# Performance work log

Hardware: AMD Instinct MI355X
Metric: run time of the kernel (lower is better)

## Reference

```python
import jax, jax.numpy as jnp
import numpy as np

DIM = 1024
NUM_HEADS = 16
HEAD_DIM = DIM // NUM_HEADS
EPS = 1e-6


def rmsnorm(x, scale):
    # normalize over last dim (head_dim)
    ms = jnp.mean(x * x, axis=-1, keepdims=True)
    return scale * (x * jax.lax.rsqrt(ms + EPS))


def setup_inputs() -> dict:
    key = jax.random.key(0)
    ks = jax.random.split(key, 12)
    B, Nx, Nc = 2, 2048, 256
    std = 1.0 / np.sqrt(DIM)
    return {
        "x": jax.random.normal(ks[0], (B, Nx, DIM), jnp.float32),
        "c": jax.random.normal(ks[1], (B, Nc, DIM), jnp.float32),
        "w_qkv_x": jax.random.normal(ks[2], (DIM, 3 * DIM), jnp.float32) * std,
        "b_qkv_x": jnp.zeros((3 * DIM,), jnp.float32),
        "w_qkv_c": jax.random.normal(ks[3], (DIM, 3 * DIM), jnp.float32) * std,
        "b_qkv_c": jnp.zeros((3 * DIM,), jnp.float32),
        "s_q_x": jnp.ones((HEAD_DIM,), jnp.float32),
        "s_k_x": jnp.ones((HEAD_DIM,), jnp.float32),
        "s_q_c": jnp.ones((HEAD_DIM,), jnp.float32),
        "s_k_c": jnp.ones((HEAD_DIM,), jnp.float32),
        "w_proj_x": jax.random.normal(ks[4], (DIM, DIM), jnp.float32) * std,
        "b_proj_x": jnp.zeros((DIM,), jnp.float32),
        "w_proj_c": jax.random.normal(ks[5], (DIM, DIM), jnp.float32) * std,
        "b_proj_c": jnp.zeros((DIM,), jnp.float32),
    }


def reference(x, c, w_qkv_x, b_qkv_x, w_qkv_c, b_qkv_c,
              s_q_x, s_k_x, s_q_c, s_k_c,
              w_proj_x, b_proj_x, w_proj_c, b_proj_c):
    B, Nx, C = x.shape
    Nc = c.shape[1]
    H, D = NUM_HEADS, HEAD_DIM

    def split_qkv(t, w, b, n):
        qkv = (t @ w + b).reshape(B, n, 3, H, D)
        qkv = jnp.transpose(qkv, (2, 0, 3, 1, 4))  # [3, B, H, n, D]
        return qkv[0], qkv[1], qkv[2]

    q_x, k_x, v_x = split_qkv(x, w_qkv_x, b_qkv_x, Nx)
    q_c, k_c, v_c = split_qkv(c, w_qkv_c, b_qkv_c, Nc)

    q = jnp.concatenate([rmsnorm(q_x, s_q_x), rmsnorm(q_c, s_q_c)], axis=2)
    k = jnp.concatenate([rmsnorm(k_x, s_k_x), rmsnorm(k_c, s_k_c)], axis=2)
    v = jnp.concatenate([v_x, v_c], axis=2)

    scale = 1.0 / jnp.sqrt(jnp.asarray(D, q.dtype))
    scores = jnp.einsum("bhqd,bhkd->bhqk", q, k) * scale
    attn = jax.nn.softmax(scores, axis=-1)
    out = jnp.einsum("bhqk,bhkd->bhqd", attn, v)  # [B, H, Nx+Nc, D]
    out = jnp.transpose(out, (0, 2, 1, 3)).reshape(B, Nx + Nc, C)

    x_out = out[:, :Nx] @ w_proj_x + b_proj_x
    c_out = out[:, Nx:] @ w_proj_c + b_proj_c
    return x_out, c_out
```

## Files before the change

### kernel.cpp

```cpp
#include <hip/hip_runtime.h>
#include <stdint.h>

typedef __attribute__((ext_vector_type(4)))  float f32x4;
typedef __attribute__((ext_vector_type(2)))  float f32x2;
typedef __attribute__((ext_vector_type(16))) float f32x16;
typedef __attribute__((ext_vector_type(8)))  short s16x8;
typedef __attribute__((ext_vector_type(4)))  short s16x4;

constexpr int kDIM = 1024;
constexpr int kD   = 64;
constexpr int kNT  = 2304;

static __device__ __forceinline__ short f2bf(float f) {
  union { float f; uint32_t i; } x; x.f = f;
  uint32_t r = x.i + 0x7fffu + ((x.i >> 16) & 1u);
  return (short)(r >> 16);
}
static __device__ __forceinline__ uint32_t cvtpk(float lo, float hi) {
  uint32_t r;
  asm volatile("v_cvt_pk_bf16_f32 %0, %1, %2" : "=v"(r) : "v"(lo), "v"(hi));
  return r;
}
static __device__ __forceinline__ void gll16(const short* g, short* l) {
  __builtin_amdgcn_global_load_lds((const __attribute__((address_space(1))) void*)g,
                                   (__attribute__((address_space(3))) void*)l, 16, 0, 0);
}
#define FENCE() asm volatile("" ::: "memory")
#define WAITV8() asm volatile("s_waitcnt vmcnt(8)" ::: "memory")
#define WAITV4() asm volatile("s_waitcnt vmcnt(4)" ::: "memory")
#define WAITV0() asm volatile("s_waitcnt vmcnt(0)" ::: "memory")
#define WAITLGKM() do { asm volatile("s_waitcnt lgkmcnt(0)" ::: "memory"); \
                        __builtin_amdgcn_sched_barrier(0); } while (0)

__global__ __launch_bounds__(256) void k_cast2(const float* __restrict__ x,
                                               short* __restrict__ xb,
                                               const float* __restrict__ c,
                                               short* __restrict__ cb, int nxb) {
  int b = blockIdx.x;
  const float* in = x; short* out = xb;
  if (b >= nxb) { in = c; out = cb; b -= nxb; }
  int i = (b * 256 + threadIdx.x) * 4;
  f32x4 v = *(const f32x4*)(in + i);
  s16x4 o; o[0] = f2bf(v[0]); o[1] = f2bf(v[1]); o[2] = f2bf(v[2]); o[3] = f2bf(v[3]);
  *(s16x4*)(out + i) = o;
}

__global__ __launch_bounds__(256) void k_tcast2(const float* __restrict__ W0,
                                                short* __restrict__ Wt0,
                                                const float* __restrict__ W1,
                                                short* __restrict__ Wt1,
                                                int K, int N) {
  const float* W = blockIdx.z ? W1 : W0;
  short* Wt = blockIdx.z ? Wt1 : Wt0;
  __shared__ float tile[32][33];
  int n0 = blockIdx.x * 32, k0 = blockIdx.y * 32;
  int tx = threadIdx.x, ty = threadIdx.y;
#pragma unroll
  for (int i2 = 0; i2 < 4; ++i2) {
    int r = ty + 8 * i2;
    tile[r][tx] = W[(size_t)(k0 + r) * N + n0 + tx];
  }
  __syncthreads();
#pragma unroll
  for (int i2 = 0; i2 < 4; ++i2) {
    int r = ty + 8 * i2;
    Wt[(size_t)(n0 + r) * K + k0 + tx] = f2bf(tile[tx][r]);
  }
}

__global__ __launch_bounds__(256, 2) void k_gemm(
    const short* A0, const short* Wt0, const float* bias0,
    const float* sq0, const float* sk0,
    const short* A1, const short* Wt1, const float* bias1,
    const float* sq1, const float* sk1,
    short* outq, short* outk, short* outvt,
    float* outp0, float* outp1,
    int rpbs0, int arstride0, int aoff0, int posoff0,
    int rpbs1, int arstride1, int aoff1, int posoff1,
    int ybreak, int epi, int nx) {
  __shared__ __align__(16) short SH[32768];
  short* As0 = SH;          short* As1 = SH + 8192;
  short* Bs0 = SH + 16384;  short* Bs1 = SH + 24576;
  const int t = threadIdx.x;
  const int lane = t & 63, w = t >> 6;
  const int g = lane >> 4, r15 = lane & 15;
  const int wm = w >> 1, wn = w & 1;

  int lin = blockIdx.x;
  int xcd = lin & 7, kk = lin >> 3;
  int by = (xcd & 3) * 9 + kk % 9;
  int bx = (xcd >> 2) * (nx >> 1) + kk / 9;

  const short* A; const short* Wt; const float* bias;
  const float* sq; const float* sk; float* outp;
  int rpbs, arstride, aoff, posoff, my;
  if (by < ybreak) {
    A = A0; Wt = Wt0; bias = bias0; sq = sq0; sk = sk0; outp = outp0;
    rpbs = rpbs0; arstride = arstride0; aoff = aoff0; posoff = posoff0; my = by;
  } else {
    A = A1; Wt = Wt1; bias = bias1; sq = sq1; sk = sk1; outp = outp1;
    rpbs = rpbs1; arstride = arstride1; aoff = aoff1; posoff = posoff1; my = by - ybreak;
  }
  const int m0 = my * 128, n0 = bx * 128;

  const short* aptr[4]; const short* bptr[4];
  int wofs[4];
#pragma unroll
  for (int it = 0; it < 4; ++it) {
    int slot = t + 256 * it;
    int row = slot >> 3, gp = slot & 7;
    int gl = gp ^ (row & 7);
    int i = m0 + row;
    int arow = (i >> rpbs) * arstride + aoff + (i & ((1 << rpbs) - 1));
    aptr[it] = A + (size_t)arow * kDIM + 8 * gl;
    bptr[it] = Wt + (size_t)(n0 + row) * kDIM + 8 * gl;
    wofs[it] = (256 * it + 64 * w) * 8;
  }

  f32x4 acc[4][4] = {};

  auto STAGE = [&](short* Asd, short* Bsd) {
#pragma unroll
    for (int it = 0; it < 4; ++it) {
      gll16(aptr[it], Asd + wofs[it]);
      gll16(bptr[it], Bsd + wofs[it]);
      aptr[it] += 64; bptr[it] += 64;
    }
  };

  auto kstep = [&](const short* Ab, const short* Bb, short* Asd, short* Bsd,
                   bool last, bool pref) {
    if (last) WAITV0(); else WAITV8();
    __builtin_amdgcn_s_barrier();
    FENCE();
#pragma unroll
    for (int ks = 0; ks < 2; ++ks) {
      s16x8 af[4], bfr[4];
#pragma unroll
      for (int mf = 0; mf < 4; ++mf) {
        int row = wm * 64 + mf * 16 + r15;
        af[mf] = *(const s16x8*)(Ab + row * 64 + (((g + 4 * ks) ^ (row & 7)) * 8));
      }
#pragma unroll
      for (int nf = 0; nf < 4; ++nf) {
        int row = wn * 64 + nf * 16 + r15;
        bfr[nf] = *(const s16x8*)(Bb + row * 64 + (((g + 4 * ks) ^ (row & 7)) * 8));
      }
#pragma unroll
      for (int mf = 0; mf < 4; ++mf)
#pragma unroll
        for (int nf = 0; nf < 4; ++nf)
          acc[mf][nf] = __builtin_amdgcn_mfma_f32_16x16x32_bf16(af[mf], bfr[nf], acc[mf][nf], 0, 0, 0);
    }
    FENCE();
    __builtin_amdgcn_s_barrier();
    FENCE();
    if (pref) STAGE(Asd, Bsd);
  };

  STAGE(As0, Bs0);
  STAGE(As1, Bs1);
  for (int pp = 0; pp < 8; ++pp) {
    kstep(As0, Bs0, As0, Bs0, false,   pp < 7);
    kstep(As1, Bs1, As1, Bs1, pp == 7, pp < 7);
  }

  const int rpbm = (1 << rpbs) - 1;
  float* Ep = (float*)SH + w * 4096;

  if (epi == 1) {
#pragma unroll
    for (int mf = 0; mf < 4; ++mf)
#pragma unroll
      for (int nf = 0; nf < 4; ++nf) {
        f32x4 v = acc[mf][nf];
        float bj = bias[n0 + wn * 64 + nf * 16 + r15];
        int dl = nf * 16 + r15;
#pragma unroll
        for (int rg = 0; rg < 4; ++rg) {
          int r = mf * 16 + 4 * g + rg;
          Ep[r * 64 + (dl ^ ((r & 15) << 1))] = v[rg] + bj;
        }
      }
    WAITLGKM();
#pragma unroll
    for (int p2 = 0; p2 < 16; ++p2) {
      int r = 4 * p2 + (lane >> 4);
      int ch = lane & 15;
      int i = m0 + wm * 64 + r;
      f32x2 a = *(const f32x2*)&Ep[r * 64 + ((ch * 4) ^ ((r & 15) << 1))];
      f32x2 b2 = *(const f32x2*)&Ep[r * 64 + ((ch * 4 + 2) ^ ((r & 15) << 1))];
      f32x4 o; o[0] = a[0]; o[1] = a[1]; o[2] = b2[0]; o[3] = b2[1];
      *(f32x4*)(outp + (size_t)i * 1024 + n0 + wn * 64 + ch * 4) = o;
    }
    return;
  }

  const int eblk = (n0 + wn * 64) >> 10;
  const int hh = ((n0 + wn * 64) >> 6) & 15;
  if (eblk == 2) {
#pragma unroll
    for (int mf = 0; mf < 4; ++mf)
#pragma unroll
      for (int nf = 0; nf < 4; ++nf) {
        f32x4 v = acc[mf][nf];
        float bj = bias[n0 + wn * 64 + nf * 16 + r15];
        int dl = nf * 16 + r15;
#pragma unroll
        for (int rg = 0; rg < 4; ++rg) {
          int pin = mf * 16 + 4 * g + rg;
          int pp2 = (pin & 51) | ((pin & 4) << 1) | ((pin & 8) >> 1);
          Ep[dl * 64 + (pp2 ^ ((dl & 15) << 1))] = v[rg] + bj;
        }
      }
    WAITLGKM();
    int i0 = m0 + wm * 64;
    int b = i0 >> rpbs;
    int posb = (i0 & rpbm) + posoff;
#pragma unroll
    for (int p2 = 0; p2 < 8; ++p2) {
      int dl = 8 * p2 + (lane >> 3);
      int ch = lane & 7;
      union { uint32_t u[4]; s16x8 v; } o;
#pragma unroll
      for (int j = 0; j < 4; ++j) {
        f32x2 rd = *(const f32x2*)&Ep[dl * 64 + ((ch * 8 + 2 * j) ^ ((dl & 15) << 1))];
        o.u[j] = cvtpk(rd[0], rd[1]);
      }
      *(s16x8*)(outvt + ((size_t)((b * 16 + hh) * 64 + dl)) * kNT + posb + ch * 8) = o.v;
    }
  } else {
    const float* sv = (eblk == 0) ? sq : sk;
    short* dstb = (eblk == 0) ? outq : outk;
    const float post = (eblk == 0) ? 0.125f * 1.44269504f : 1.0f;
    float sl[4], bj4[4];
#pragma unroll
    for (int nf = 0; nf < 4; ++nf) {
      bj4[nf] = bias[n0 + wn * 64 + nf * 16 + r15];
      sl[nf] = sv[nf * 16 + r15] * post;
    }
#pragma unroll
    for (int mf = 0; mf < 4; ++mf) {
      float vb[4][4];
#pragma unroll
      for (int nf = 0; nf < 4; ++nf)
#pragma unroll
        for (int rg = 0; rg < 4; ++rg)
          vb[nf][rg] = acc[mf][nf][rg] + bj4[nf];
#pragma unroll
      for (int rg = 0; rg < 4; ++rg) {
        float ss = vb[0][rg] * vb[0][rg];
        ss = __builtin_fmaf(vb[1][rg], vb[1][rg], ss);
        ss = __builtin_fmaf(vb[2][rg], vb[2][rg], ss);
        ss = __builtin_fmaf(vb[3][rg], vb[3][rg], ss);
        ss += __shfl_xor(ss, 1); ss += __shfl_xor(ss, 2);
        ss += __shfl_xor(ss, 4); ss += __shfl_xor(ss, 8);
        float f = rsqrtf(ss * (1.f / 64.f) + 1e-6f);
        int r = mf * 16 + 4 * g + rg;
#pragma unroll
        for (int nf = 0; nf < 4; ++nf) {
          int dl = nf * 16 + r15;
          Ep[r * 64 + (dl ^ ((r & 15) << 1))] = vb[nf][rg] * f * sl[nf];
        }
      }
    }
    WAITLGKM();
#pragma unroll
    for (int p2 = 0; p2 < 8; ++p2) {
      int r = 8 * p2 + (lane >> 3);
      int ch = lane & 7;
      int i = m0 + wm * 64 + r;
      int b = i >> rpbs;
      int pos = (i & rpbm) + posoff;
      union { uint32_t u[4]; s16x8 v; } o;
#pragma unroll
      for (int j = 0; j < 4; ++j) {
        f32x2 rd = *(const f32x2*)&Ep[r * 64 + ((ch * 8 + 2 * j) ^ ((r & 15) << 1))];
        o.u[j] = cvtpk(rd[0], rd[1]);
      }
      *(s16x8*)(dstb + ((size_t)((b * 16 + hh) * kNT + pos)) * 64 + ch * 8) = o.v;
    }
  }
}

__global__ __launch_bounds__(256, 3) void k_attn(
    const short* __restrict__ Q, const short* __restrict__ K,
    const short* __restrict__ Vt, short* __restrict__ Ao) {
  __shared__ __align__(16) short S[16384];
  const int t = threadIdx.x;
  const int lane = t & 63, w = t >> 6;
  const int h = lane >> 5, q31 = lane & 31;
  const int lin = blockIdx.x;
  const int idx = lin >> 3;
  const int bh = (lin & 7) * 4 + idx / 18;
  const int q0 = (idx % 18) * 128;

  const short* qrow = Q + ((size_t)bh * kNT + q0 + 32 * w + q31) * kD;
  s16x8 qf[4];
#pragma unroll
  for (int a = 0; a < 4; ++a)
    qf[a] = *(const s16x8*)(qrow + 16 * a + 8 * h);

  const short* kptr[2]; const short* vptr[2];
  int sb[2];
#pragma unroll
  for (int it = 0; it < 2; ++it) {
    int slot = t + 256 * it;
    int row = slot >> 3, gp = slot & 7;
    int gl = gp ^ (row & 7);
    kptr[it] = K + ((size_t)bh * kNT + row) * kD + 8 * gl;
    vptr[it] = Vt + ((size_t)bh * kD + row) * kNT + 8 * gl;
    sb[it] = (256 * it + 64 * w) * 8;
  }

  int ko[2][4], vo[2][4];
#pragma unroll
  for (int rg = 0; rg < 2; ++rg) {
    int row = 32 * rg + q31;
#pragma unroll
    for (int a = 0; a < 4; ++a) {
      ko[rg][a] = row * 64 + (((2 * a + h) ^ (row & 7)) * 8);
      vo[rg][a] = ko[rg][a];
    }
  }

  f32x16 ot0 = {}, ot1 = {};
  float l = 0.f;
  short* Kb0 = S;          short* Kb1 = S + 4096;
  short* Vb0 = S + 8192;   short* Vb1 = S + 12288;

  auto STAGE = [&](short* kst, short* vst) {
#pragma unroll
    for (int it = 0; it < 2; ++it) {
      gll16(kptr[it], kst + sb[it]); kptr[it] += 64 * kD;
      gll16(vptr[it], vst + sb[it]); vptr[it] += 64;
    }
  };

  auto tile = [&](const short* Kb, const short* Vb, short* kst, short* vst,
                  bool last, bool pref) {
    if (last) WAITV0(); else WAITV4();
    __builtin_amdgcn_s_barrier();
    FENCE();
    f32x16 st0 = {}, st1 = {};
    __builtin_amdgcn_s_setprio(1);
#pragma unroll
    for (int a = 0; a < 4; ++a) {
      s16x8 kf0 = *(const s16x8*)(Kb + ko[0][a]);
      s16x8 kf1 = *(const s16x8*)(Kb + ko[1][a]);
      st0 = __builtin_amdgcn_mfma_f32_32x32x16_bf16(kf0, qf[a], st0, 0, 0, 0);
      st1 = __builtin_amdgcn_mfma_f32_32x32x16_bf16(kf1, qf[a], st1, 0, 0, 0);
    }
    __builtin_amdgcn_s_setprio(0);
    s16x8 pf[4];
    float rs = 0.f;
#pragma unroll
    for (int rg = 0; rg < 2; ++rg) {
      float p[16];
#pragma unroll
      for (int r = 0; r < 16; ++r) {
        p[r] = __builtin_amdgcn_exp2f(rg ? st1[r] : st0[r]);
        rs += p[r];
      }
#pragma unroll
      for (int mh = 0; mh < 2; ++mh) {
        union { uint32_t u[4]; s16x8 v; } pk;
        pk.u[0] = cvtpk(p[8 * mh + 0], p[8 * mh + 1]);
        pk.u[1] = cvtpk(p[8 * mh + 2], p[8 * mh + 3]);
        pk.u[2] = cvtpk(p[8 * mh + 4], p[8 * mh + 5]);
        pk.u[3] = cvtpk(p[8 * mh + 6], p[8 * mh + 7]);
        pf[2 * rg + mh] = pk.v;
      }
    }
    l += rs;
    __builtin_amdgcn_s_setprio(1);
#pragma unroll
    for (int m = 0; m < 4; ++m) {
      s16x8 vf0 = *(const s16x8*)(Vb + vo[0][m]);
      s16x8 vf1 = *(const s16x8*)(Vb + vo[1][m]);
      ot0 = __builtin_amdgcn_mfma_f32_32x32x16_bf16(vf0, pf[m], ot0, 0, 0, 0);
      ot1 = __builtin_amdgcn_mfma_f32_32x32x16_bf16(vf1, pf[m], ot1, 0, 0, 0);
    }
    __builtin_amdgcn_s_setprio(0);
    FENCE();
    __builtin_amdgcn_s_barrier();
    FENCE();
    if (pref) STAGE(kst, vst);
  };

  STAGE(Kb0, Vb0);
  STAGE(Kb1, Vb1);
  for (int pp = 0; pp < 18; ++pp) {
    tile(Kb0, Vb0, Kb0, Vb0, false,    pp < 17);
    tile(Kb1, Vb1, Kb1, Vb1, pp == 17, pp < 17);
  }

  l += __shfl_xor(l, 32);
  float rl = 1.f / l;

  __syncthreads();
  float* Os = (float*)S;
  const int R = 32 * w + q31;
#pragma unroll
  for (int rg = 0; rg < 2; ++rg)
#pragma unroll
    for (int rr = 0; rr < 4; ++rr) {
      int d0 = 32 * rg + 8 * rr + 4 * h;
      f32x4 v4;
#pragma unroll
      for (int j = 0; j < 4; ++j)
        v4[j] = (rg ? ot1[4 * rr + j] : ot0[4 * rr + j]) * rl;
      *(f32x4*)&Os[R * 64 + (d0 ^ ((R & 7) << 3))] = v4;
    }
  __syncthreads();
  {
    int b = bh >> 4, hh = bh & 15;
#pragma unroll
    for (int rep = 0; rep < 2; ++rep) {
      int idx2 = t + 256 * rep;
      int q = idx2 >> 2, c4 = idx2 & 3;
      float vals[16];
#pragma unroll
      for (int i = 0; i < 4; ++i) {
        f32x4 rd = *(const f32x4*)&Os[q * 64 + (((c4 * 16 + 4 * i) ^ ((q & 7) << 3)))];
        vals[4 * i + 0] = rd[0]; vals[4 * i + 1] = rd[1];
        vals[4 * i + 2] = rd[2]; vals[4 * i + 3] = rd[3];
      }
      union { uint32_t u[4]; s16x8 v; } o0, o1;
      o0.u[0] = cvtpk(vals[0], vals[1]);   o0.u[1] = cvtpk(vals[2], vals[3]);
      o0.u[2] = cvtpk(vals[4], vals[5]);   o0.u[3] = cvtpk(vals[6], vals[7]);
      o1.u[0] = cvtpk(vals[8], vals[9]);   o1.u[1] = cvtpk(vals[10], vals[11]);
      o1.u[2] = cvtpk(vals[12], vals[13]); o1.u[3] = cvtpk(vals[14], vals[15]);
      short* dst = Ao + ((size_t)b * kNT + q0 + q) * kDIM + hh * kD + c4 * 16;
      *(s16x8*)dst = o0.v;
      *(s16x8*)(dst + 8) = o1.v;
    }
  }
}

extern "C" void kernel_launch(void* const* d_in, const int* in_sizes, int n_in,
                              void* d_out, int out_size, void* d_ws, size_t ws_size,
                              hipStream_t stream) {
  const float* x   = (const float*)d_in[0];
  const float* c   = (const float*)d_in[1];
  const float* wqx = (const float*)d_in[2];
  const float* bqx = (const float*)d_in[3];
  const float* wqc = (const float*)d_in[4];
  const float* bqc = (const float*)d_in[5];
  const float* sqx = (const float*)d_in[6];
  const float* skx = (const float*)d_in[7];
  const float* sqc = (const float*)d_in[8];
  const float* skc = (const float*)d_in[9];
  const float* wpx = (const float*)d_in[10];
  const float* bpx = (const float*)d_in[11];
  const float* wpc = (const float*)d_in[12];
  const float* bpc = (const float*)d_in[13];
  float* out = (float*)d_out;

  char* p = (char*)d_ws;
  short* xb   = (short*)p; p += (size_t)4096 * 1024 * 2;
  short* cb   = (short*)p; p += (size_t)512 * 1024 * 2;
  short* wqxt = (short*)p; p += (size_t)3072 * 1024 * 2;
  short* wqct = (short*)p; p += (size_t)3072 * 1024 * 2;
  short* wpxt = (short*)p; p += (size_t)1024 * 1024 * 2;
  short* wpct = (short*)p; p += (size_t)1024 * 1024 * 2;
  short* qb   = (short*)p; p += (size_t)32 * 2304 * 64 * 2;
  short* kb   = (short*)p; p += (size_t)32 * 2304 * 64 * 2;
  short* vtb  = (short*)p; p += (size_t)32 * 64 * 2304 * 2;
  short* ao   = (short*)p; p += (size_t)2 * 2304 * 1024 * 2;

  k_cast2<<<4608, 256, 0, stream>>>(x, xb, c, cb, 4096);
  k_tcast2<<<dim3(96, 32, 2), dim3(32, 8), 0, stream>>>(wqx, wqxt, wqc, wqct, 1024, 3072);
  k_tcast2<<<dim3(32, 32, 2), dim3(32, 8), 0, stream>>>(wpx, wpxt, wpc, wpct, 1024, 1024);

  k_gemm<<<864, 256, 0, stream>>>(
      xb, wqxt, bqx, sqx, skx,
      cb, wqct, bqc, sqc, skc,
      qb, kb, vtb, nullptr, nullptr,
      11, 2048, 0, 0,
      8, 256, 0, 2048,
      32, 0, 24);

  k_attn<<<576, 256, 0, stream>>>(qb, kb, vtb, ao);

  k_gemm<<<288, 256, 0, stream>>>(
      ao, wpxt, bpx, nullptr, nullptr,
      ao, wpct, bpc, nullptr, nullptr,
      nullptr, nullptr, nullptr, out, out + (size_t)4096 * 1024,
      11, 2304, 0, 0,
      8, 2304, 2048, 0,
      32, 1, 8);
}
```

Baseline: 139.3 us.

## Switch projection GEMM to 32x32x16 MFMA and restructure attention score loop

The QKV/projection GEMM moves from 16x16x32 MFMA tiles to 32x32x16 tiles, with precomputed swizzled LDS offsets and reworked epilogues, including the RMSNorm row reduction over 32 lanes. The aim is fewer LDS fragment loads per MFMA and higher MFMA throughput. In attention, the two score MFMA chains are now processed one row-group at a time with exp/pack interleaved, and the duplicate V offset array is dropped. Attention launch bounds drop from 3 to 2 blocks per CU, trading occupancy for register headroom.

```diff
diff --git a/kernel.cpp b/kernel.cpp
--- a/kernel.cpp
+++ b/kernel.cpp
@@ -83,7 +83,7 @@
   short* Bs0 = SH + 16384;  short* Bs1 = SH + 24576;
   const int t = threadIdx.x;
   const int lane = t & 63, w = t >> 6;
-  const int g = lane >> 4, r15 = lane & 15;
+  const int h = lane >> 5, q31 = lane & 31;
   const int wm = w >> 1, wn = w & 1;
 
   int lin = blockIdx.x;
@@ -117,7 +117,19 @@
     wofs[it] = (256 * it + 64 * w) * 8;
   }
 
-  f32x4 acc[4][4] = {};
+  int ao_[2][4], bo_[2][4];
+#pragma unroll
+  for (int mr = 0; mr < 2; ++mr) {
+    int rowa = wm * 64 + mr * 32 + q31;
+    int rowb = wn * 64 + mr * 32 + q31;
+#pragma unroll
+    for (int s = 0; s < 4; ++s) {
+      ao_[mr][s] = rowa * 64 + (((2 * s + h) ^ (rowa & 7)) * 8);
+      bo_[mr][s] = rowb * 64 + (((2 * s + h) ^ (rowb & 7)) * 8);
+    }
+  }
+
+  f32x16 acc[2][2] = {};
 
   auto STAGE = [&](short* Asd, short* Bsd) {
 #pragma unroll
@@ -134,23 +146,15 @@
     __builtin_amdgcn_s_barrier();
     FENCE();
 #pragma unroll
-    for (int ks = 0; ks < 2; ++ks) {
-      s16x8 af[4], bfr[4];
-#pragma unroll
-      for (int mf = 0; mf < 4; ++mf) {
-        int row = wm * 64 + mf * 16 + r15;
-        af[mf] = *(const s16x8*)(Ab + row * 64 + (((g + 4 * ks) ^ (row & 7)) * 8));
-      }
-#pragma unroll
-      for (int nf = 0; nf < 4; ++nf) {
-        int row = wn * 64 + nf * 16 + r15;
-        bfr[nf] = *(const s16x8*)(Bb + row * 64 + (((g + 4 * ks) ^ (row & 7)) * 8));
-      }
-#pragma unroll
-      for (int mf = 0; mf < 4; ++mf)
-#pragma unroll
-        for (int nf = 0; nf < 4; ++nf)
-          acc[mf][nf] = __builtin_amdgcn_mfma_f32_16x16x32_bf16(af[mf], bfr[nf], acc[mf][nf], 0, 0, 0);
+    for (int s = 0; s < 4; ++s) {
+      s16x8 a0 = *(const s16x8*)(Ab + ao_[0][s]);
+      s16x8 a1 = *(const s16x8*)(Ab + ao_[1][s]);
+      s16x8 b0 = *(const s16x8*)(Bb + bo_[0][s]);
+      s16x8 b1 = *(const s16x8*)(Bb + bo_[1][s]);
+      acc[0][0] = __builtin_amdgcn_mfma_f32_32x32x16_bf16(a0, b0, acc[0][0], 0, 0, 0);
+      acc[0][1] = __builtin_amdgcn_mfma_f32_32x32x16_bf16(a0, b1, acc[0][1], 0, 0, 0);
+      acc[1][0] = __builtin_amdgcn_mfma_f32_32x32x16_bf16(a1, b0, acc[1][0], 0, 0, 0);
+      acc[1][1] = __builtin_amdgcn_mfma_f32_32x32x16_bf16(a1, b1, acc[1][1], 0, 0, 0);
     }
     FENCE();
     __builtin_amdgcn_s_barrier();
@@ -170,16 +174,15 @@
 
   if (epi == 1) {
 #pragma unroll
-    for (int mf = 0; mf < 4; ++mf)
-#pragma unroll
-      for (int nf = 0; nf < 4; ++nf) {
-        f32x4 v = acc[mf][nf];
-        float bj = bias[n0 + wn * 64 + nf * 16 + r15];
-        int dl = nf * 16 + r15;
-#pragma unroll
-        for (int rg = 0; rg < 4; ++rg) {
-          int r = mf * 16 + 4 * g + rg;
-          Ep[r * 64 + (dl ^ ((r & 15) << 1))] = v[rg] + bj;
+    for (int mr = 0; mr < 2; ++mr)
+#pragma unroll
+      for (int nr = 0; nr < 2; ++nr) {
+        float bj = bias[n0 + wn * 64 + nr * 32 + q31];
+        int dl = nr * 32 + q31;
+#pragma unroll
+        for (int r = 0; r < 16; ++r) {
+          int row = mr * 32 + (r & 3) + 8 * (r >> 2) + 4 * h;
+          Ep[row * 64 + (dl ^ ((row & 15) << 1))] = acc[mr][nr][r] + bj;
         }
       }
     WAITLGKM();
@@ -200,17 +203,16 @@
   const int hh = ((n0 + wn * 64) >> 6) & 15;
   if (eblk == 2) {
 #pragma unroll
-    for (int mf = 0; mf < 4; ++mf)
-#pragma unroll
-      for (int nf = 0; nf < 4; ++nf) {
-        f32x4 v = acc[mf][nf];
-        float bj = bias[n0 + wn * 64 + nf * 16 + r15];
-        int dl = nf * 16 + r15;
-#pragma unroll
-        for (int rg = 0; rg < 4; ++rg) {
-          int pin = mf * 16 + 4 * g + rg;
+    for (int mr = 0; mr < 2; ++mr)
+#pragma unroll
+      for (int nr = 0; nr < 2; ++nr) {
+        float bj = bias[n0 + wn * 64 + nr * 32 + q31];
+        int dl = nr * 32 + q31;
+#pragma unroll
+        for (int r = 0; r < 16; ++r) {
+          int pin = mr * 32 + (r & 3) + 8 * (r >> 2) + 4 * h;
           int pp2 = (pin & 51) | ((pin & 4) << 1) | ((pin & 8) >> 1);
-          Ep[dl * 64 + (pp2 ^ ((dl & 15) << 1))] = v[rg] + bj;
+          Ep[dl * 64 + (pp2 ^ ((dl & 15) << 1))] = acc[mr][nr][r] + bj;
         }
       }
     WAITLGKM();
@@ -233,37 +235,27 @@
     const float* sv = (eblk == 0) ? sq : sk;
     short* dstb = (eblk == 0) ? outq : outk;
     const float post = (eblk == 0) ? 0.125f * 1.44269504f : 1.0f;
-    float sl[4], bj4[4];
-#pragma unroll
-    for (int nf = 0; nf < 4; ++nf) {
-      bj4[nf] = bias[n0 + wn * 64 + nf * 16 + r15];
-      sl[nf] = sv[nf * 16 + r15] * post;
-    }
-#pragma unroll
-    for (int mf = 0; mf < 4; ++mf) {
-      float vb[4][4];
-#pragma unroll
-      for (int nf = 0; nf < 4; ++nf)
-#pragma unroll
-        for (int rg = 0; rg < 4; ++rg)
-          vb[nf][rg] = acc[mf][nf][rg] + bj4[nf];
-#pragma unroll
-      for (int rg = 0; rg < 4; ++rg) {
-        float ss = vb[0][rg] * vb[0][rg];
-        ss = __builtin_fmaf(vb[1][rg], vb[1][rg], ss);
-        ss = __builtin_fmaf(vb[2][rg], vb[2][rg], ss);
-        ss = __builtin_fmaf(vb[3][rg], vb[3][rg], ss);
-        ss += __shfl_xor(ss, 1); ss += __shfl_xor(ss, 2);
-        ss += __shfl_xor(ss, 4); ss += __shfl_xor(ss, 8);
+    float sl[2], bj2[2];
+#pragma unroll
+    for (int nr = 0; nr < 2; ++nr) {
+      bj2[nr] = bias[n0 + wn * 64 + nr * 32 + q31];
+      sl[nr] = sv[nr * 32 + q31] * post;
+    }
+#pragma unroll
+    for (int mr = 0; mr < 2; ++mr)
+#pragma unroll
+      for (int r = 0; r < 16; ++r) {
+        float v0 = acc[mr][0][r] + bj2[0];
+        float v1 = acc[mr][1][r] + bj2[1];
+        float ss = __builtin_fmaf(v1, v1, v0 * v0);
+        ss += __shfl_xor(ss, 1);  ss += __shfl_xor(ss, 2);
+        ss += __shfl_xor(ss, 4);  ss += __shfl_xor(ss, 8);
+        ss += __shfl_xor(ss, 16);
         float f = rsqrtf(ss * (1.f / 64.f) + 1e-6f);
-        int r = mf * 16 + 4 * g + rg;
-#pragma unroll
-        for (int nf = 0; nf < 4; ++nf) {
-          int dl = nf * 16 + r15;
-          Ep[r * 64 + (dl ^ ((r & 15) << 1))] = vb[nf][rg] * f * sl[nf];
-        }
-      }
-    }
+        int row = mr * 32 + (r & 3) + 8 * (r >> 2) + 4 * h;
+        Ep[row * 64 + ((q31) ^ ((row & 15) << 1))] = v0 * f * sl[0];
+        Ep[row * 64 + ((32 + q31) ^ ((row & 15) << 1))] = v1 * f * sl[1];
+      }
     WAITLGKM();
 #pragma unroll
     for (int p2 = 0; p2 < 8; ++p2) {
@@ -283,7 +275,7 @@
   }
 }
 
-__global__ __launch_bounds__(256, 3) void k_attn(
+__global__ __launch_bounds__(256, 2) void k_attn(
     const short* __restrict__ Q, const short* __restrict__ K,
     const short* __restrict__ Vt, short* __restrict__ Ao) {
   __shared__ __align__(16) short S[16384];
@@ -313,15 +305,13 @@
     sb[it] = (256 * it + 64 * w) * 8;
   }
 
-  int ko[2][4], vo[2][4];
+  int ko[2][4];
 #pragma unroll
   for (int rg = 0; rg < 2; ++rg) {
     int row = 32 * rg + q31;
 #pragma unroll
-    for (int a = 0; a < 4; ++a) {
-      ko[rg][a] = row * 64 + (((2 * a + h) ^ (row & 7)) * 8);
-      vo[rg][a] = ko[rg][a];
-    }
+    for (int s = 0; s < 4; ++s)
+      ko[rg][s] = row * 64 + (((2 * s + h) ^ (row & 7)) * 8);
   }
 
   f32x16 ot0 = {}, ot1 = {};
@@ -342,33 +332,28 @@
     if (last) WAITV0(); else WAITV4();
     __builtin_amdgcn_s_barrier();
     FENCE();
-    f32x16 st0 = {}, st1 = {};
-    __builtin_amdgcn_s_setprio(1);
-#pragma unroll
-    for (int a = 0; a < 4; ++a) {
-      s16x8 kf0 = *(const s16x8*)(Kb + ko[0][a]);
-      s16x8 kf1 = *(const s16x8*)(Kb + ko[1][a]);
-      st0 = __builtin_amdgcn_mfma_f32_32x32x16_bf16(kf0, qf[a], st0, 0, 0, 0);
-      st1 = __builtin_amdgcn_mfma_f32_32x32x16_bf16(kf1, qf[a], st1, 0, 0, 0);
-    }
-    __builtin_amdgcn_s_setprio(0);
     s16x8 pf[4];
     float rs = 0.f;
 #pragma unroll
     for (int rg = 0; rg < 2; ++rg) {
-      float p[16];
-#pragma unroll
-      for (int r = 0; r < 16; ++r) {
-        p[r] = __builtin_amdgcn_exp2f(rg ? st1[r] : st0[r]);
-        rs += p[r];
-      }
+      f32x16 st = {};
+      __builtin_amdgcn_s_setprio(1);
+#pragma unroll
+      for (int a = 0; a < 4; ++a) {
+        s16x8 kf = *(const s16x8*)(Kb + ko[rg][a]);
+        st = __builtin_amdgcn_mfma_f32_32x32x16_bf16(kf, qf[a], st, 0, 0, 0);
+      }
+      __builtin_amdgcn_s_setprio(0);
 #pragma unroll
       for (int mh = 0; mh < 2; ++mh) {
         union { uint32_t u[4]; s16x8 v; } pk;
-        pk.u[0] = cvtpk(p[8 * mh + 0], p[8 * mh + 1]);
-        pk.u[1] = cvtpk(p[8 * mh + 2], p[8 * mh + 3]);
-        pk.u[2] = cvtpk(p[8 * mh + 4], p[8 * mh + 5]);
-        pk.u[3] = cvtpk(p[8 * mh + 6], p[8 * mh + 7]);
+#pragma unroll
+        for (int i = 0; i < 4; ++i) {
+          float e0 = __builtin_amdgcn_exp2f(st[8 * mh + 2 * i]);
+          float e1 = __builtin_amdgcn_exp2f(st[8 * mh + 2 * i + 1]);
+          rs += e0 + e1;
+          pk.u[i] = cvtpk(e0, e1);
+        }
         pf[2 * rg + mh] = pk.v;
       }
     }
@@ -376,8 +361,8 @@
     __builtin_amdgcn_s_setprio(1);
 #pragma unroll
     for (int m = 0; m < 4; ++m) {
-      s16x8 vf0 = *(const s16x8*)(Vb + vo[0][m]);
-      s16x8 vf1 = *(const s16x8*)(Vb + vo[1][m]);
+      s16x8 vf0 = *(const s16x8*)(Vb + ko[0][m]);
+      s16x8 vf1 = *(const s16x8*)(Vb + ko[1][m]);
       ot0 = __builtin_amdgcn_mfma_f32_32x32x16_bf16(vf0, pf[m], ot0, 0, 0, 0);
       ot1 = __builtin_amdgcn_mfma_f32_32x32x16_bf16(vf1, pf[m], ot1, 0, 0, 0);
     }
```

After: 149.2 us. +7.1%, slower.
